# Kernel optimization log

Measured on AMD Instinct MI355X. Metric: run time of the kernel, lower is better.

Reference implementation:

```python
import jax, jax.numpy as jnp
import numpy as np

# 8-neighborhood offsets (dy, dx) in the same order as the torch module,
# so bit i of the LBP code corresponds to offsets[i].
OFFSETS = ((-1, -1), (-1, 0), (-1, 1), (0, 1), (1, 1), (1, 0), (1, -1), (0, -1))
NUM_BINS = 256


def setup_inputs() -> dict:
    key = jax.random.key(0)
    x = jax.random.uniform(key, (64, 3, 512, 512), dtype=jnp.float32)
    return {"x": x}


def reference(x) -> jnp.ndarray:
    bs, _, H, W = x.shape
    # RGB -> grayscale, [bs, H, W]
    gray = 0.2989 * x[:, 0] + 0.587 * x[:, 1] + 0.114 * x[:, 2]
    # replicate-pad by 1 on each spatial side ('edge' == torch 'replicate')
    pad = jnp.pad(gray, ((0, 0), (1, 1), (1, 1)), mode="edge")

    # Accumulate the 8-bit LBP code directly (fuses the codes/weights pass).
    lbp = jnp.zeros((bs, H, W), dtype=jnp.int32)
    for i, (dy, dx) in enumerate(OFFSETS):
        neigh = pad[:, 1 + dy:1 + dy + H, 1 + dx:1 + dx + W]
        lbp = lbp + (neigh >= gray).astype(jnp.int32) * (1 << i)

    # 256-bin histogram per image via a single scatter-add (bincount-style),
    # replacing the O(256*H*W) looped equality sums of the original.
    batch_idx = jnp.arange(bs, dtype=jnp.int32)[:, None]          # [bs, 1]
    flat = lbp.reshape(bs, H * W)                                  # [bs, H*W]
    hist = jnp.zeros((bs, NUM_BINS), dtype=jnp.float32).at[batch_idx, flat].add(1.0)

    # L2-normalize each histogram.
    norm = jnp.sqrt(jnp.sum(hist * hist, axis=1, keepdims=True))
    return hist / (norm + 1e-6)
```

## Files before the change

kernel.cpp:

```cpp
#include <hip/hip_runtime.h>

#define IMG_H 512
#define IMG_W 512
#define PLANE (IMG_H * IMG_W)
#define NBATCH 64
#define NBINS 256
#define TSTRIP 8
#define WAVES_PER_BLOCK 4
#define STRIPS_PER_IMG (IMG_H / TSTRIP)
#define BLOCKS_PER_IMG (STRIPS_PER_IMG / WAVES_PER_BLOCK)
#define NBLOCKS (BLOCKS_PER_IMG * NBATCH)

#define GRAY(rr, gg, bb) (0.2989f * (rr) + 0.587f * (gg) + 0.114f * (bb))

__global__ __launch_bounds__(256) void lbp_strip_kernel(const float* __restrict__ x,
                                                        float* __restrict__ ws) {
    __shared__ unsigned int lh[NBINS];
    const int tid = threadIdx.x;
    lh[tid] = 0u;
    __syncthreads();

    const int lin = blockIdx.x;
    const int sid = (lin & 7) * (NBLOCKS / 8) + (lin >> 3);
    const int b   = sid >> 4;
    const int bg  = sid & 15;

    const int wav   = tid >> 6;
    const int lane  = tid & 63;
    const int strip = bg * WAVES_PER_BLOCK + wav;
    const int y0    = strip * TSTRIP;

    const float* rP = x + (size_t)b * 3 * PLANE;
    const float* gP = rP + PLANE;
    const float* bP = rP + 2 * PLANE;
    const int    cx = 8 * lane;

    float t_[10], m_[10], b_[10];

    #define LOADGRAY(arr, gy_)                                                     \
    do {                                                                           \
        int gy = (gy_);                                                            \
        gy = gy < 0 ? 0 : (gy > IMG_H - 1 ? IMG_H - 1 : gy);                       \
        size_t off = (size_t)gy * IMG_W + cx;                                      \
        float4 ra = *(const float4*)(rP + off), rb = *(const float4*)(rP + off + 4);\
        float4 ga = *(const float4*)(gP + off), gb = *(const float4*)(gP + off + 4);\
        float4 ba = *(const float4*)(bP + off), bb = *(const float4*)(bP + off + 4);\
        arr[1] = GRAY(ra.x, ga.x, ba.x); arr[2] = GRAY(ra.y, ga.y, ba.y);          \
        arr[3] = GRAY(ra.z, ga.z, ba.z); arr[4] = GRAY(ra.w, ga.w, ba.w);          \
        arr[5] = GRAY(rb.x, gb.x, bb.x); arr[6] = GRAY(rb.y, gb.y, bb.y);          \
        arr[7] = GRAY(rb.z, gb.z, bb.z); arr[8] = GRAY(rb.w, gb.w, bb.w);          \
        float lft = __shfl_up(arr[8], 1, 64);                                      \
        float rgt = __shfl_down(arr[1], 1, 64);                                    \
        arr[0] = (lane == 0)  ? arr[1] : lft;                                      \
        arr[9] = (lane == 63) ? arr[8] : rgt;                                      \
    } while (0)

    #define COMPUTE8()                                                             \
    do {                                                                           \
        _Pragma("unroll")                                                          \
        for (int p = 0; p < 8; ++p) {                                              \
            const float ctr = m_[p + 1];                                           \
            unsigned code = 0u;                                                    \
            code |= (t_[p    ] >= ctr) ? 1u   : 0u;                                \
            code |= (t_[p + 1] >= ctr) ? 2u   : 0u;                                \
            code |= (t_[p + 2] >= ctr) ? 4u   : 0u;                                \
            code |= (m_[p + 2] >= ctr) ? 8u   : 0u;                                \
            code |= (b_[p + 2] >= ctr) ? 16u  : 0u;                                \
            code |= (b_[p + 1] >= ctr) ? 32u  : 0u;                                \
            code |= (b_[p    ] >= ctr) ? 64u  : 0u;                                \
            code |= (m_[p    ] >= ctr) ? 128u : 0u;                                \
            atomicAdd(&lh[code], 1u);                                              \
        }                                                                          \
    } while (0)

    if ((strip & 1) == 0) {
        LOADGRAY(t_, y0 - 1);
        LOADGRAY(m_, y0);
        #pragma unroll
        for (int i = 0; i < TSTRIP; ++i) {
            LOADGRAY(b_, y0 + 1 + i);
            COMPUTE8();
            #pragma unroll
            for (int k = 0; k < 10; ++k) { t_[k] = m_[k]; m_[k] = b_[k]; }
        }
    } else {
        LOADGRAY(b_, y0 + TSTRIP);
        LOADGRAY(m_, y0 + TSTRIP - 1);
        #pragma unroll
        for (int i = 0; i < TSTRIP; ++i) {
            LOADGRAY(t_, y0 + TSTRIP - 2 - i);
            COMPUTE8();
            #pragma unroll
            for (int k = 0; k < 10; ++k) { b_[k] = m_[k]; m_[k] = t_[k]; }
        }
    }
    #undef LOADGRAY
    #undef COMPUTE8

    __syncthreads();
    ws[((size_t)b * BLOCKS_PER_IMG + bg) * NBINS + tid] = (float)lh[tid];
}

__global__ __launch_bounds__(256) void finalize_kernel(const float* __restrict__ ws,
                                                       float* __restrict__ out) {
    const int b = blockIdx.x;
    const int t = threadIdx.x;
    float s = 0.0f;
    #pragma unroll
    for (int k = 0; k < BLOCKS_PER_IMG; ++k)
        s += ws[((size_t)b * BLOCKS_PER_IMG + k) * NBINS + t];
    float ss = s * s;
    #pragma unroll
    for (int o = 32; o > 0; o >>= 1) ss += __shfl_down(ss, o, 64);
    __shared__ float wsum[4];
    if ((t & 63) == 0) wsum[t >> 6] = ss;
    __syncthreads();
    float tot = wsum[0] + wsum[1] + wsum[2] + wsum[3];
    out[b * NBINS + t] = s / (sqrtf(tot) + 1e-6f);
}

extern "C" void kernel_launch(void* const* d_in, const int* in_sizes, int n_in,
                              void* d_out, int out_size, void* d_ws, size_t ws_size,
                              hipStream_t stream) {
    const float* x = (const float*)d_in[0];
    float* out = (float*)d_out;
    float* ws  = (float*)d_ws;

    lbp_strip_kernel<<<NBLOCKS, 256, 0, stream>>>(x, ws);
    finalize_kernel<<<NBATCH, 256, 0, stream>>>(ws, out);
}
```

Measured before the change: 40.60 us.

## Split rows into half-width wave tiles and build LBP code via cmp/addc asm

```diff
diff --git a/kernel.cpp b/kernel.cpp
--- a/kernel.cpp
+++ b/kernel.cpp
@@ -5,10 +5,10 @@
 #define PLANE (IMG_H * IMG_W)
 #define NBATCH 64
 #define NBINS 256
-#define TSTRIP 8
-#define WAVES_PER_BLOCK 4
-#define STRIPS_PER_IMG (IMG_H / TSTRIP)
-#define BLOCKS_PER_IMG (STRIPS_PER_IMG / WAVES_PER_BLOCK)
+#define TSTRIP 16
+#define HALF_W 256
+#define WPB 4
+#define BLOCKS_PER_IMG 16
 #define NBLOCKS (BLOCKS_PER_IMG * NBATCH)
 
 #define GRAY(rr, gg, bb) (0.2989f * (rr) + 0.587f * (gg) + 0.114f * (bb))
@@ -27,48 +27,54 @@
 
     const int wav   = tid >> 6;
     const int lane  = tid & 63;
-    const int strip = bg * WAVES_PER_BLOCK + wav;
+    const int strip = bg * 2 + (wav >> 1);
+    const int half  = wav & 1;
     const int y0    = strip * TSTRIP;
 
     const float* rP = x + (size_t)b * 3 * PLANE;
     const float* gP = rP + PLANE;
     const float* bP = rP + 2 * PLANE;
-    const int    cx = 8 * lane;
+    const int    cx = half * HALF_W + 4 * lane;
 
-    float t_[10], m_[10], b_[10];
+    float t_[6], m_[6], b_[6];
 
     #define LOADGRAY(arr, gy_)                                                     \
     do {                                                                           \
         int gy = (gy_);                                                            \
         gy = gy < 0 ? 0 : (gy > IMG_H - 1 ? IMG_H - 1 : gy);                       \
         size_t off = (size_t)gy * IMG_W + cx;                                      \
-        float4 ra = *(const float4*)(rP + off), rb = *(const float4*)(rP + off + 4);\
-        float4 ga = *(const float4*)(gP + off), gb = *(const float4*)(gP + off + 4);\
-        float4 ba = *(const float4*)(bP + off), bb = *(const float4*)(bP + off + 4);\
+        float4 ra = *(const float4*)(rP + off);                                    \
+        float4 ga = *(const float4*)(gP + off);                                    \
+        float4 ba = *(const float4*)(bP + off);                                    \
         arr[1] = GRAY(ra.x, ga.x, ba.x); arr[2] = GRAY(ra.y, ga.y, ba.y);          \
         arr[3] = GRAY(ra.z, ga.z, ba.z); arr[4] = GRAY(ra.w, ga.w, ba.w);          \
-        arr[5] = GRAY(rb.x, gb.x, bb.x); arr[6] = GRAY(rb.y, gb.y, bb.y);          \
-        arr[7] = GRAY(rb.z, gb.z, bb.z); arr[8] = GRAY(rb.w, gb.w, bb.w);          \
-        float lft = __shfl_up(arr[8], 1, 64);                                      \
-        float rgt = __shfl_down(arr[1], 1, 64);                                    \
-        arr[0] = (lane == 0)  ? arr[1] : lft;                                      \
-        arr[9] = (lane == 63) ? arr[8] : rgt;                                      \
+        arr[0] = __shfl_up(arr[4], 1, 64);                                         \
+        arr[5] = __shfl_down(arr[1], 1, 64);                                       \
+        if (lane == 0)                                                             \
+            arr[0] = half ? GRAY(rP[off - 1], gP[off - 1], bP[off - 1]) : arr[1];  \
+        if (lane == 63)                                                            \
+            arr[5] = half ? arr[4] : GRAY(rP[off + 4], gP[off + 4], bP[off + 4]);  \
     } while (0)
 
-    #define COMPUTE8()                                                             \
+    #define LBPBIT(nei)                                                            \
+        asm volatile("v_cmp_ge_f32 vcc, %1, %2\n\t"                                \
+                     "v_addc_co_u32 %0, vcc, %0, %0, vcc"                          \
+                     : "+v"(code) : "v"(nei), "v"(ctr) : "vcc")
+
+    #define COMPUTE4()                                                             \
     do {                                                                           \
         _Pragma("unroll")                                                          \
-        for (int p = 0; p < 8; ++p) {                                              \
+        for (int p = 0; p < 4; ++p) {                                              \
             const float ctr = m_[p + 1];                                           \
             unsigned code = 0u;                                                    \
-            code |= (t_[p    ] >= ctr) ? 1u   : 0u;                                \
-            code |= (t_[p + 1] >= ctr) ? 2u   : 0u;                                \
-            code |= (t_[p + 2] >= ctr) ? 4u   : 0u;                                \
-            code |= (m_[p + 2] >= ctr) ? 8u   : 0u;                                \
-            code |= (b_[p + 2] >= ctr) ? 16u  : 0u;                                \
-            code |= (b_[p + 1] >= ctr) ? 32u  : 0u;                                \
-            code |= (b_[p    ] >= ctr) ? 64u  : 0u;                                \
-            code |= (m_[p    ] >= ctr) ? 128u : 0u;                                \
+            LBPBIT(m_[p    ]);                                            \
+            LBPBIT(b_[p    ]);                                            \
+            LBPBIT(b_[p + 1]);                                            \
+            LBPBIT(b_[p + 2]);                                            \
+            LBPBIT(m_[p + 2]);                                            \
+            LBPBIT(t_[p + 2]);                                            \
+            LBPBIT(t_[p + 1]);                                            \
+            LBPBIT(t_[p    ]);                                            \
             atomicAdd(&lh[code], 1u);                                              \
         }                                                                          \
     } while (0)
@@ -79,9 +85,9 @@
         #pragma unroll
         for (int i = 0; i < TSTRIP; ++i) {
             LOADGRAY(b_, y0 + 1 + i);
-            COMPUTE8();
+            COMPUTE4();
             #pragma unroll
-            for (int k = 0; k < 10; ++k) { t_[k] = m_[k]; m_[k] = b_[k]; }
+            for (int k = 0; k < 6; ++k) { t_[k] = m_[k]; m_[k] = b_[k]; }
         }
     } else {
         LOADGRAY(b_, y0 + TSTRIP);
@@ -89,13 +95,14 @@
         #pragma unroll
         for (int i = 0; i < TSTRIP; ++i) {
             LOADGRAY(t_, y0 + TSTRIP - 2 - i);
-            COMPUTE8();
+            COMPUTE4();
             #pragma unroll
-            for (int k = 0; k < 10; ++k) { b_[k] = m_[k]; m_[k] = t_[k]; }
+            for (int k = 0; k < 6; ++k) { b_[k] = m_[k]; m_[k] = t_[k]; }
         }
     }
     #undef LOADGRAY
-    #undef COMPUTE8
+    #undef LBPBIT
+    #undef COMPUTE4
 
     __syncthreads();
     ws[((size_t)b * BLOCKS_PER_IMG + bg) * NBINS + tid] = (float)lh[tid];
```

After: 37.56 us (median of 2 runs). -7.5%, faster.
